# Optimization experiments

Measured on AMD Instinct MI355X. Metric: run time of the kernel, lower is better.

## Reference

```python
import jax, jax.numpy as jnp
import numpy as np

BS, C_IN, H, W = 16, 128, 64, 64
C_OUT, K, STRIDE, PAD, DIL = 256, 3, 1, 1, 1
ALPHA = 0.5  # scaling_factor
QMAX = 127.0  # int8 symmetric fake-quant


def _fake_quant(t):
    # symmetric per-tensor int8 fake quantization with straight-through estimator
    s = jax.lax.stop_gradient(jnp.max(jnp.abs(t))) / QMAX
    s = jnp.where(s == 0, 1.0, s)
    q = jnp.clip(jnp.round(t / s), -QMAX, QMAX) * s
    return t + jax.lax.stop_gradient(q - t)  # STE


def setup_inputs() -> dict:
    key = jax.random.key(0)
    k1, k2, k3 = jax.random.split(key, 3)
    x = jax.random.normal(k1, (BS, C_IN, H, W), dtype=jnp.float32)
    weight = jax.random.normal(k2, (C_OUT, C_IN, K, K), dtype=jnp.float32) * 0.05
    bias = jax.random.normal(k3, (C_OUT,), dtype=jnp.float32) * 0.01
    return {"x": x, "weight": weight, "bias": bias}


def reference(x, weight, bias):
    bs, _, h_in, w_in = x.shape
    ickhkw = C_IN * K * K
    h_out = (h_in + 2 * PAD - DIL * (K - 1) - 1) // STRIDE + 1
    w_out = (w_in + 2 * PAD - DIL * (K - 1) - 1) // STRIDE + 1

    # im2col (matches torch F.unfold feature ordering: channel-major, then kh, kw)
    patches = jax.lax.conv_general_dilated_patches(
        x, filter_shape=(K, K), window_strides=(STRIDE, STRIDE),
        padding=((PAD, PAD), (PAD, PAD)), rhs_dilation=(DIL, DIL),
    )  # [bs, ickhkw, h_out, w_out]
    cols = patches.reshape(bs, ickhkw, h_out * w_out)
    cols = cols.transpose(0, 2, 1).reshape(-1, ickhkw)  # [bs*L, ickhkw]

    w2 = weight.reshape(C_OUT, ickhkw)

    # SmoothQuant per-column scales (detached)
    w_scale = jax.lax.stop_gradient(jnp.max(jnp.abs(w2), axis=0))    # [ickhkw]
    act_scale = jax.lax.stop_gradient(jnp.max(jnp.abs(cols), axis=0))  # [ickhkw]
    scale = act_scale ** ALPHA / w_scale ** (1.0 - ALPHA)
    scale = jnp.where(scale == 0, 1.0, scale)

    w_s = _fake_quant(w2 * scale)
    x_s = _fake_quant(cols / scale)

    out = x_s @ w_s.T  # [bs*L, C_OUT]
    out = out.reshape(bs, h_out * w_out, C_OUT).transpose(0, 2, 1)
    out = out.reshape(bs, C_OUT, h_out, w_out)
    return out + bias.reshape(1, C_OUT, 1, 1)
```

## Files before the change

### kernel.cpp

```cpp
#include <hip/hip_runtime.h>
#include <cstdint>

#define C_IN   128
#define C_OUT  256
#define KK     1152
#define NPIX   4096
#define BS     16
#define M_ROWS 65536
#define QMAXF  127.0f

typedef int v4i __attribute__((ext_vector_type(4)));
typedef float f4 __attribute__((ext_vector_type(4)));

#define OFF_QW    75497472
#define OFF_SCALE 75792384
#define OFF_QMUL  75796992
#define OFF_APART 75801600
#define OFF_SCAL  75843072

__global__ void k_prep(const float* __restrict__ x, const float* __restrict__ wgt,
                       float* __restrict__ act_part, float* __restrict__ w_part) {
    const int tid = threadIdx.x;
    if (blockIdx.x >= 1024) {
        int t = blockIdx.x - 1024;
        int j = (t % 5) * 256 + tid;
        int s = t / 5;
        if (j >= KK) return;
        const float* p = wgt + (size_t)s * 16 * KK + j;
        float m = 0.f;
#pragma unroll
        for (int i = 0; i < 16; i++) m = fmaxf(m, fabsf(p[(size_t)i * KK]));
        w_part[s * KK + j] = m;
        return;
    }
    const int c = blockIdx.x >> 3, s = blockIdx.x & 7;
    float m[9];
#pragma unroll
    for (int i = 0; i < 9; i++) m[i] = 0.f;
    for (int p = tid; p < 2 * NPIX; p += 256) {
        int b = s * 2 + (p >> 12);
        int hw = p & 4095;
        int h = hw >> 6, w = hw & 63;
        float v = fabsf(x[b * (C_IN * NPIX) + c * NPIX + hw]);
        bool rr[3] = { h <= 62, true, h >= 1 };
        bool cc[3] = { w <= 62, true, w >= 1 };
#pragma unroll
        for (int i = 0; i < 3; i++)
#pragma unroll
            for (int jq = 0; jq < 3; jq++)
                m[i * 3 + jq] = fmaxf(m[i * 3 + jq], (rr[i] && cc[jq]) ? v : 0.f);
    }
    __shared__ float sm[9][4];
    int lane = tid & 63, wid = tid >> 6;
#pragma unroll
    for (int i = 0; i < 9; i++) {
        float v = m[i];
        for (int off = 32; off > 0; off >>= 1) v = fmaxf(v, __shfl_down(v, off));
        if (lane == 0) sm[i][wid] = v;
    }
    __syncthreads();
    if (tid < 9) {
        float v = fmaxf(fmaxf(sm[tid][0], sm[tid][1]), fmaxf(sm[tid][2], sm[tid][3]));
        act_part[s * KK + c * 9 + tid] = v;
    }
}

__global__ void k_scales(const float* __restrict__ act_part, const float* __restrict__ w_part,
                         float* __restrict__ scale, float* __restrict__ qmul,
                         float* __restrict__ scalars) {
    const int tid = threadIdx.x;
    float sc_local[2] = {1.f, 1.f};
    float mx = 0.f, mw = 0.f;
#pragma unroll
    for (int t = 0; t < 2; t++) {
        int j = tid + t * 1024;
        if (j < KK) {
            float a = 0.f;
#pragma unroll
            for (int s = 0; s < 8; s++) a = fmaxf(a, act_part[s * KK + j]);
            float wv = 0.f;
#pragma unroll
            for (int s = 0; s < 16; s++) wv = fmaxf(wv, w_part[s * KK + j]);
            float sc = sqrtf(a) / sqrtf(wv);
            if (sc == 0.f) sc = 1.0f;
            scale[j] = sc;
            sc_local[t] = sc;
            mx = fmaxf(mx, a / sc);
            mw = fmaxf(mw, wv * sc);
        }
    }
    __shared__ float smx[16], smw[16];
    __shared__ float s_x_sh;
    int lane = tid & 63, wid = tid >> 6;
    for (int off = 32; off > 0; off >>= 1) {
        mx = fmaxf(mx, __shfl_down(mx, off));
        mw = fmaxf(mw, __shfl_down(mw, off));
    }
    if (lane == 0) { smx[wid] = mx; smw[wid] = mw; }
    __syncthreads();
    if (tid == 0) {
        float a = 0.f, b = 0.f;
        for (int i = 0; i < 16; i++) { a = fmaxf(a, smx[i]); b = fmaxf(b, smw[i]); }
        float s_x = a / QMAXF; if (s_x == 0.f) s_x = 1.f;
        float s_w = b / QMAXF; if (s_w == 0.f) s_w = 1.f;
        scalars[0] = s_x; scalars[1] = s_w; scalars[2] = s_x * s_w;
        s_x_sh = s_x;
    }
    __syncthreads();
    float s_x = s_x_sh;
#pragma unroll
    for (int t = 0; t < 2; t++) {
        int j = tid + t * 1024;
        if (j < KK) qmul[j] = 1.0f / (sc_local[t] * s_x);
    }
}

__global__ void k_quant_w(const float* __restrict__ wgt, const float* __restrict__ scale,
                          const float* __restrict__ scalars, signed char* __restrict__ qWp) {
    int idx = blockIdx.x * 256 + threadIdx.x;
    int m  = (unsigned)idx / KK;
    int kp = idx - m * KK;
    int tap = kp >> 7, c = kp & 127;
    int j = c * 9 + tap;
    float s_w = scalars[1];
    float t = wgt[m * KK + j] * scale[j];
    float q = rintf(t / s_w);
    q = fminf(fmaxf(q, -QMAXF), QMAXF);
    qWp[idx] = (signed char)(int)q;
}

__global__ __launch_bounds__(512) void k_gemm(const signed char* __restrict__ qWp,
                                              const float* __restrict__ x,
                                              const float* __restrict__ qmul,
                                              const float* __restrict__ scalars,
                                              const float* __restrict__ bias,
                                              float* __restrict__ out) {
    __shared__ __align__(16) signed char As[256 * 128];
    __shared__ __align__(16) signed char Bs[128 * 128];
    __shared__ float qm[KK];
    const int tid = threadIdx.x;
    const int lane = tid & 63, wv = tid >> 6;
    const int wm = wv & 3, wn = wv >> 2;
    const int b   = blockIdx.x >> 5;
    const int rp  = blockIdx.x & 31;
    const int oh0 = rp * 2;
    const float* xb = x + (size_t)b * (C_IN * NPIX);

    for (int i = tid; i < KK; i += 512) {
        int tap = i >> 7, c = i & 127;
        qm[i] = qmul[c * 9 + tap];
    }

    const int r8 = lane >> 3;
    const int cpA = (lane & 7) ^ r8;
    const int ohl = wv & 1;
    const int px  = ohl * 64 + lane;
    const int swz = lane & 7;
    const int oh  = oh0 + ohl;

    v4i acc[4][4];
#pragma unroll
    for (int i = 0; i < 4; i++)
#pragma unroll
        for (int jq = 0; jq < 4; jq++) acc[i][jq] = (v4i){0, 0, 0, 0};

    __syncthreads();

    for (int tap = 0; tap < 9; tap++) {
        const int kh = (tap * 11) >> 5;
        const int kw = tap - kh * 3;
        const int ih = oh + kh - 1;
        const bool rowok = (unsigned)ih < 64u;
#pragma unroll
        for (int i = 0; i < 4; i++) {
            int ch = wv * 4 + i;
            const signed char* src = qWp + (size_t)(ch * 8 + r8) * KK + tap * 128 + cpA * 16;
            __builtin_amdgcn_global_load_lds(
                (const __attribute__((address_space(1))) void*)src,
                (__attribute__((address_space(3))) void*)(As + ch * 1024), 16, 0, 0);
        }
        const int iw = lane + kw - 1;
        const bool colok = (unsigned)iw < 64u;
        const float* srow = xb + ih * 64 + iw;
#pragma unroll
        for (int j = 0; j < 2; j++) {
            int cc = j * 4 + (wv >> 1);
            int c0 = cc * 16;
            int pk[4];
#pragma unroll
            for (int d = 0; d < 4; d++) {
                f4 qv = *(const f4*)(qm + tap * 128 + c0 + d * 4);
                int w = 0;
#pragma unroll
                for (int e = 0; e < 4; e++) {
                    int c = c0 + d * 4 + e;
                    float v = (rowok && colok) ? srow[(size_t)c * NPIX] : 0.f;
                    float q = rintf(v * qv[e]);
                    q = fminf(fmaxf(q, -QMAXF), QMAXF);
                    w |= ((int)q & 255) << (8 * e);
                }
                pk[d] = w;
            }
            *(v4i*)(Bs + px * 128 + ((cc ^ swz) * 16)) = (v4i){pk[0], pk[1], pk[2], pk[3]};
        }
        __syncthreads();
#pragma unroll
        for (int h = 0; h < 2; h++) {
            const int q4 = h * 4 + (lane >> 4);
            v4i af[4], bf[4];
#pragma unroll
            for (int t = 0; t < 4; t++) {
                int ra = wm * 64 + t * 16 + (lane & 15);
                af[t] = *(const v4i*)(As + ra * 128 + ((q4 ^ (ra & 7)) * 16));
                int rb = wn * 64 + t * 16 + (lane & 15);
                bf[t] = *(const v4i*)(Bs + rb * 128 + ((q4 ^ (rb & 7)) * 16));
            }
#pragma unroll
            for (int mt = 0; mt < 4; mt++)
#pragma unroll
                for (int nt = 0; nt < 4; nt++)
                    acc[mt][nt] = __builtin_amdgcn_mfma_i32_16x16x64_i8(af[mt], bf[nt], acc[mt][nt], 0, 0, 0);
        }
        __syncthreads();
    }

    const float ssp = scalars[2];
    const int quad = lane >> 4, col = lane & 15;
    float bv[4][4];
#pragma unroll
    for (int mt = 0; mt < 4; mt++)
#pragma unroll
        for (int rg = 0; rg < 4; rg++)
            bv[mt][rg] = bias[wm * 64 + mt * 16 + quad * 4 + rg];

#pragma unroll
    for (int mt = 0; mt < 4; mt++) {
#pragma unroll
        for (int nt = 0; nt < 4; nt++) {
            int n = wn * 64 + nt * 16 + col;
#pragma unroll
            for (int rg = 0; rg < 4; rg++) {
                int m = wm * 64 + mt * 16 + quad * 4 + rg;
                float v = (float)acc[mt][nt][rg] * ssp + bv[mt][rg];
                out[(size_t)(b * C_OUT + m) * NPIX + oh0 * 64 + n] = v;
            }
        }
    }
}

extern "C" void kernel_launch(void* const* d_in, const int* in_sizes, int n_in,
                              void* d_out, int out_size, void* d_ws, size_t ws_size,
                              hipStream_t stream) {
    const float* x    = (const float*)d_in[0];
    const float* wgt  = (const float*)d_in[1];
    const float* bias = (const float*)d_in[2];
    float* out = (float*)d_out;

    char* ws = (char*)d_ws;
    signed char* qWp = (signed char*)(ws + OFF_QW);
    float* w_part    = (float*)(ws + OFF_QW);
    float* scale     = (float*)(ws + OFF_SCALE);
    float* qmul      = (float*)(ws + OFF_QMUL);
    float* act_part  = (float*)(ws + OFF_APART);
    float* scalars   = (float*)(ws + OFF_SCAL);

    k_prep<<<1104, 256, 0, stream>>>(x, wgt, act_part, w_part);
    k_scales<<<1, 1024, 0, stream>>>(act_part, w_part, scale, qmul, scalars);
    k_quant_w<<<(C_OUT * KK) / 256, 256, 0, stream>>>(wgt, scale, scalars, qWp);
    k_gemm<<<BS * 32, 512, 0, stream>>>(qWp, x, qmul, scalars, bias, out);
}
```

Baseline: 164.2 us.

## Restructure int8 GEMM: register-resident weights, double-buffered B tile, prefetch next tap

The conv GEMM kernel now uses 256-thread blocks, each covering one output row of 64 pixels, twice as many blocks as before. Weight fragments are loaded straight from global memory into registers rather than staged through LDS. The quantized activation tile is double-buffered in LDS, which removes one barrier per tap. The next tap's weights and activations are prefetched into registers while the current tap's MFMAs run, to hide global load latency. The cost is much higher register pressure (32 floats plus 16 vectors of prefetch) and weight reuse only within one block, which means more global and L2 weight traffic.

```diff
diff --git a/kernel.cpp b/kernel.cpp
--- a/kernel.cpp
+++ b/kernel.cpp
@@ -10,7 +10,6 @@
 #define QMAXF  127.0f
 
 typedef int v4i __attribute__((ext_vector_type(4)));
-typedef float f4 __attribute__((ext_vector_type(4)));
 
 #define OFF_QW    75497472
 #define OFF_SCALE 75792384
@@ -129,34 +128,51 @@
     qWp[idx] = (signed char)(int)q;
 }
 
-__global__ __launch_bounds__(512) void k_gemm(const signed char* __restrict__ qWp,
-                                              const float* __restrict__ x,
-                                              const float* __restrict__ qmul,
-                                              const float* __restrict__ scalars,
-                                              const float* __restrict__ bias,
-                                              float* __restrict__ out) {
-    __shared__ __align__(16) signed char As[256 * 128];
-    __shared__ __align__(16) signed char Bs[128 * 128];
+__device__ __forceinline__ void load_xv(const float* __restrict__ xb, int oh, int tap,
+                                        int lane, int c0a, int c0b, float* xv) {
+    const int kh = (tap * 11) >> 5;
+    const int kw = tap - kh * 3;
+    const int ih = oh + kh - 1;
+    const int iw = lane + kw - 1;
+    const bool ok = ((unsigned)ih < 64u) && ((unsigned)iw < 64u);
+    const float* s = xb + ih * 64 + iw;
+#pragma unroll
+    for (int d = 0; d < 16; d++) xv[d]      = ok ? s[(size_t)(c0a + d) * NPIX] : 0.f;
+#pragma unroll
+    for (int d = 0; d < 16; d++) xv[16 + d] = ok ? s[(size_t)(c0b + d) * NPIX] : 0.f;
+}
+
+__device__ __forceinline__ void load_af(const signed char* __restrict__ aBase, int tap,
+                                        v4i af[2][4]) {
+#pragma unroll
+    for (int h = 0; h < 2; h++)
+#pragma unroll
+        for (int mt = 0; mt < 4; mt++)
+            af[h][mt] = *(const v4i*)(aBase + (size_t)mt * 16 * KK + tap * 128 + h * 64);
+}
+
+__global__ __launch_bounds__(256, 2) void k_gemm(const signed char* __restrict__ qWp,
+                                                 const float* __restrict__ x,
+                                                 const float* __restrict__ qmul,
+                                                 const float* __restrict__ scalars,
+                                                 const float* __restrict__ bias,
+                                                 float* __restrict__ out) {
+    __shared__ __align__(16) signed char Bs[2][64 * 128];
     __shared__ float qm[KK];
     const int tid = threadIdx.x;
     const int lane = tid & 63, wv = tid >> 6;
-    const int wm = wv & 3, wn = wv >> 2;
-    const int b   = blockIdx.x >> 5;
-    const int rp  = blockIdx.x & 31;
-    const int oh0 = rp * 2;
+    const int b  = blockIdx.x >> 6;
+    const int oh = blockIdx.x & 63;
     const float* xb = x + (size_t)b * (C_IN * NPIX);
 
-    for (int i = tid; i < KK; i += 512) {
+    for (int i = tid; i < KK; i += 256) {
         int tap = i >> 7, c = i & 127;
         qm[i] = qmul[c * 9 + tap];
     }
 
-    const int r8 = lane >> 3;
-    const int cpA = (lane & 7) ^ r8;
-    const int ohl = wv & 1;
-    const int px  = ohl * 64 + lane;
+    const signed char* aBase = qWp + (size_t)(wv * 64 + (lane & 15)) * KK + (lane >> 4) * 16;
+    const int c0a = wv * 16, c0b = (wv + 4) * 16;
     const int swz = lane & 7;
-    const int oh  = oh0 + ohl;
 
     v4i acc[4][4];
 #pragma unroll
@@ -164,64 +180,65 @@
 #pragma unroll
         for (int jq = 0; jq < 4; jq++) acc[i][jq] = (v4i){0, 0, 0, 0};
 
-    __syncthreads();
-
+    v4i af[2][4];
+    float xv[32];
+    load_af(aBase, 0, af);
+    load_xv(xb, oh, 0, lane, c0a, c0b, xv);
+
+    __syncthreads();
+
+#pragma unroll
     for (int tap = 0; tap < 9; tap++) {
-        const int kh = (tap * 11) >> 5;
-        const int kw = tap - kh * 3;
-        const int ih = oh + kh - 1;
-        const bool rowok = (unsigned)ih < 64u;
-#pragma unroll
-        for (int i = 0; i < 4; i++) {
-            int ch = wv * 4 + i;
-            const signed char* src = qWp + (size_t)(ch * 8 + r8) * KK + tap * 128 + cpA * 16;
-            __builtin_amdgcn_global_load_lds(
-                (const __attribute__((address_space(1))) void*)src,
-                (__attribute__((address_space(3))) void*)(As + ch * 1024), 16, 0, 0);
-        }
-        const int iw = lane + kw - 1;
-        const bool colok = (unsigned)iw < 64u;
-        const float* srow = xb + ih * 64 + iw;
-#pragma unroll
-        for (int j = 0; j < 2; j++) {
-            int cc = j * 4 + (wv >> 1);
-            int c0 = cc * 16;
-            int pk[4];
-#pragma unroll
-            for (int d = 0; d < 4; d++) {
-                f4 qv = *(const f4*)(qm + tap * 128 + c0 + d * 4);
-                int w = 0;
-#pragma unroll
-                for (int e = 0; e < 4; e++) {
-                    int c = c0 + d * 4 + e;
-                    float v = (rowok && colok) ? srow[(size_t)c * NPIX] : 0.f;
-                    float q = rintf(v * qv[e]);
-                    q = fminf(fmaxf(q, -QMAXF), QMAXF);
-                    w |= ((int)q & 255) << (8 * e);
-                }
-                pk[d] = w;
+        signed char* bsp = Bs[tap & 1];
+        const float* qmt = qm + tap * 128;
+        int pk[8];
+#pragma unroll
+        for (int d = 0; d < 8; d++) {
+            int w = 0;
+            int cbase = (d < 4) ? (c0a + d * 4) : (c0b + (d - 4) * 4);
+#pragma unroll
+            for (int e = 0; e < 4; e++) {
+                float q = rintf(xv[d * 4 + e] * qmt[cbase + e]);
+                q = fminf(fmaxf(q, -QMAXF), QMAXF);
+                w |= ((int)q & 255) << (8 * e);
             }
-            *(v4i*)(Bs + px * 128 + ((cc ^ swz) * 16)) = (v4i){pk[0], pk[1], pk[2], pk[3]};
-        }
+            pk[d] = w;
+        }
+        *(v4i*)(bsp + lane * 128 + ((wv ^ swz) * 16))       = (v4i){pk[0], pk[1], pk[2], pk[3]};
+        *(v4i*)(bsp + lane * 128 + (((wv + 4) ^ swz) * 16)) = (v4i){pk[4], pk[5], pk[6], pk[7]};
         __syncthreads();
+
+        v4i afn[2][4];
+        float xvn[32];
+        if (tap < 8) {
+            load_af(aBase, tap + 1, afn);
+            load_xv(xb, oh, tap + 1, lane, c0a, c0b, xvn);
+        }
+
 #pragma unroll
         for (int h = 0; h < 2; h++) {
             const int q4 = h * 4 + (lane >> 4);
-            v4i af[4], bf[4];
-#pragma unroll
-            for (int t = 0; t < 4; t++) {
-                int ra = wm * 64 + t * 16 + (lane & 15);
-                af[t] = *(const v4i*)(As + ra * 128 + ((q4 ^ (ra & 7)) * 16));
-                int rb = wn * 64 + t * 16 + (lane & 15);
-                bf[t] = *(const v4i*)(Bs + rb * 128 + ((q4 ^ (rb & 7)) * 16));
+            v4i bf[4];
+#pragma unroll
+            for (int nt = 0; nt < 4; nt++) {
+                int rb = nt * 16 + (lane & 15);
+                bf[nt] = *(const v4i*)(bsp + rb * 128 + ((q4 ^ (rb & 7)) * 16));
             }
 #pragma unroll
             for (int mt = 0; mt < 4; mt++)
 #pragma unroll
                 for (int nt = 0; nt < 4; nt++)
-                    acc[mt][nt] = __builtin_amdgcn_mfma_i32_16x16x64_i8(af[mt], bf[nt], acc[mt][nt], 0, 0, 0);
-        }
-        __syncthreads();
+                    acc[mt][nt] = __builtin_amdgcn_mfma_i32_16x16x64_i8(af[h][mt], bf[nt], acc[mt][nt], 0, 0, 0);
+        }
+
+        if (tap < 8) {
+#pragma unroll
+            for (int h = 0; h < 2; h++)
+#pragma unroll
+                for (int mt = 0; mt < 4; mt++) af[h][mt] = afn[h][mt];
+#pragma unroll
+            for (int i = 0; i < 32; i++) xv[i] = xvn[i];
+        }
     }
 
     const float ssp = scalars[2];
@@ -231,18 +248,18 @@
     for (int mt = 0; mt < 4; mt++)
 #pragma unroll
         for (int rg = 0; rg < 4; rg++)
-            bv[mt][rg] = bias[wm * 64 + mt * 16 + quad * 4 + rg];
-
+            bv[mt][rg] = bias[wv * 64 + mt * 16 + quad * 4 + rg];
+
+    float* obase = out + ((size_t)b * C_OUT) * NPIX + oh * 64;
 #pragma unroll
     for (int mt = 0; mt < 4; mt++) {
 #pragma unroll
         for (int nt = 0; nt < 4; nt++) {
-            int n = wn * 64 + nt * 16 + col;
+            int n = nt * 16 + col;
 #pragma unroll
             for (int rg = 0; rg < 4; rg++) {
-                int m = wm * 64 + mt * 16 + quad * 4 + rg;
-                float v = (float)acc[mt][nt][rg] * ssp + bv[mt][rg];
-                out[(size_t)(b * C_OUT + m) * NPIX + oh0 * 64 + n] = v;
+                int m = wv * 64 + mt * 16 + quad * 4 + rg;
+                obase[(size_t)m * NPIX + n] = (float)acc[mt][nt][rg] * ssp + bv[mt][rg];
             }
         }
     }
@@ -267,5 +284,5 @@
     k_prep<<<1104, 256, 0, stream>>>(x, wgt, act_part, w_part);
     k_scales<<<1, 1024, 0, stream>>>(act_part, w_part, scale, qmul, scalars);
     k_quant_w<<<(C_OUT * KK) / 256, 256, 0, stream>>>(wgt, scale, scalars, qWp);
-    k_gemm<<<BS * 32, 512, 0, stream>>>(qWp, x, qmul, scalars, bias, out);
-}
+    k_gemm<<<BS * 64, 256, 0, stream>>>(qWp, x, qmul, scalars, bias, out);
+}
```

After: 223.6 us. 36.1% more time.
